# Performance work log

Measured on AMD Instinct MI355X. Metric: run time of the kernel, lower is better.

Reference implementation:

```python
import jax, jax.numpy as jnp
import numpy as np

B, CIN, COUT, N, TIN = 8, 64, 64, 207, 54
K, NHID, SL, KT = 8, 64, 3, 3
HEADS, STRIDE, PL = 8, 4, 8
TIME_NUM, OUT_LEN = 120, 48
E = COUT * PL            # 512 = attention embed dim (embed_size*patch_len)
PD = E // HEADS          # 64 per-head dim
PNUM = (OUT_LEN + STRIDE - PL) // STRIDE + 1   # 12 patches
EPS = 1e-5


def setup_inputs():
    keys = iter(jax.random.split(jax.random.key(0), 48))
    def rn(shape, s):
        return jax.random.normal(next(keys), shape, jnp.float32) * s
    d = {}
    d['x'] = rn((B, CIN, N, TIN), 1.0)
    d['adj'] = jax.random.uniform(next(keys), (SL, N, N), jnp.float32) / N
    d['W_conv1'] = rn((COUT, CIN), 0.125); d['b_conv1'] = rn((COUT,), 0.02)
    d['g_T'] = jnp.ones((TIN,), jnp.float32); d['b_T'] = jnp.zeros((TIN,), jnp.float32)
    d['g_S'] = jnp.ones((N,), jnp.float32); d['b_S'] = jnp.zeros((N,), jnp.float32)
    d['W_time'] = rn((2*COUT, 3*COUT, 1, KT), 1.0/np.sqrt(3*COUT*KT)); d['b_time'] = rn((2*COUT,), 0.02)
    d['wq1'] = rn((SL, K, COUT, NHID), 0.125); d['wv1'] = rn((SL, K, COUT, NHID), 0.125)
    d['bias1'] = rn((SL, NHID), 0.05)
    d['wq2'] = rn((SL, K, NHID, 2*COUT), 0.125); d['wv2'] = rn((SL, K, NHID, 2*COUT), 0.125)
    d['bias2'] = rn((SL, 2*COUT), 0.05)
    d['W_mlp'] = rn((2*COUT, SL*2*COUT, 1, KT), 1.0/np.sqrt(SL*2*COUT*KT)); d['b_mlp'] = rn((2*COUT,), 0.02)
    d['emb_T'] = rn((TIME_NUM, E), 0.02)
    d['Wq'] = rn((PD, PD), 0.125); d['bq'] = rn((PD,), 0.02)
    d['Wk'] = rn((PD, PD), 0.125); d['bk'] = rn((PD,), 0.02)
    d['Wv'] = rn((PD, PD), 0.125); d['bv'] = rn((PD,), 0.02)
    d['W_fc'] = rn((E, E), 1.0/np.sqrt(E)); d['b_fc'] = rn((E,), 0.02)
    d['g1'] = jnp.ones((E,), jnp.float32); d['b1n'] = jnp.zeros((E,), jnp.float32)
    d['g2'] = jnp.ones((E,), jnp.float32); d['b2n'] = jnp.zeros((E,), jnp.float32)
    d['W_ff1'] = rn((E, 4*COUT), 1.0/np.sqrt(E)); d['b_ff1'] = rn((4*COUT,), 0.02)
    d['W_ff2'] = rn((4*COUT, E), 1.0/np.sqrt(4*COUT)); d['b_ff2'] = rn((E,), 0.02)
    d['W_rp'] = rn((PNUM*PL, OUT_LEN), 1.0/np.sqrt(PNUM*PL)); d['b_rp'] = rn((OUT_LEN,), 0.02)
    d['g_bn'] = jnp.ones((COUT,), jnp.float32); d['b_bn'] = jnp.zeros((COUT,), jnp.float32)
    return d


def _ln(v, g, b, axis):
    m = jnp.mean(v, axis=axis, keepdims=True)
    var = jnp.var(v, axis=axis, keepdims=True)
    xhat = (v - m) * jax.lax.rsqrt(var + EPS)
    shp = [1] * v.ndim; shp[axis] = -1
    return xhat * g.reshape(shp) + b.reshape(shp)


def _gconv(x, wq, wv, bias, a):
    # x: [B,C,N,L]; wq/wv: [K,C,D]; a: [N,N]  -- multi-basis sigmoid-gated GCN
    q = jnp.einsum('bcnl,kcd->kbdnl', x, wq)
    v = jnp.einsum('bcnl,kcd->kbdnl', x, wv)
    s = jnp.sum(jax.nn.sigmoid(q) * v, axis=0)           # [B,D,N,L]
    out = jnp.einsum('nk,bcnl->bckl', a, s)              # adjacency aggregation (exact index order of source)
    return out + bias[None, :, None, None]


def _conv2d(x, w, b, dil):
    y = jax.lax.conv_general_dilated(x, w, (1, 1), 'VALID', rhs_dilation=(1, dil),
                                     dimension_numbers=('NCHW', 'OIHW', 'NCHW'))
    return y + b[None, :, None, None]


def reference(x, adj, W_conv1, b_conv1, g_T, b_T, g_S, b_S, W_time, b_time,
              wq1, wv1, bias1, wq2, wv2, bias2, W_mlp, b_mlp, emb_T,
              Wq, bq, Wk, bk, Wv, bv, W_fc, b_fc, g1, b1n, g2, b2n,
              W_ff1, b_ff1, W_ff2, b_ff2, W_rp, b_rp, g_bn, b_bn):
    residual = jnp.einsum('oc,bcnl->bonl', W_conv1, x) + b_conv1[None, :, None, None]
    xcat = jnp.concatenate([residual, _ln(residual, g_T, b_T, 3), _ln(residual, g_S, b_S, 2)], axis=1)
    h = _conv2d(xcat, W_time, b_time, 2)                 # [B,2C,N,50]
    h = jnp.tanh(h[:, :COUT]) * jax.nn.sigmoid(h[:, COUT:])
    outs = [_gconv(jax.nn.relu(_gconv(h, wq1[i], wv1[i], bias1[i], adj[i])),
                   wq2[i], wv2[i], bias2[i], adj[i]) for i in range(SL)]
    g = _conv2d(jnp.concatenate(outs, axis=1), W_mlp, b_mlp, 1)   # [B,2C,N,48]
    g = jnp.tanh(g[:, :COUT]) * jax.nn.sigmoid(g[:, COUT:])      # [B,C,N,48]
    # --- TTransformer with patching ---
    z = jnp.pad(g, ((0, 0), (0, 0), (0, 0), (0, STRIDE)))        # pad time by stride (52 >= patch_len)
    idx = jnp.arange(PNUM)[:, None] * STRIDE + jnp.arange(PL)[None, :]
    patches = z[..., idx]                                        # [B,C,N,P,PL] unfold
    q0 = patches.reshape(B, N, PNUM, E)                          # row-major reshape, as in torch source
    xe = q0 + emb_T[:PNUM][None, None]
    qh = xe.reshape(B, N, PNUM, HEADS, PD)
    qs = qh @ Wq + bq; ks = qh @ Wk + bk; vs = qh @ Wv + bv
    scores = jnp.einsum('bnqhd,bnkhd->bnqkh', qs, ks)
    att = jax.nn.softmax(scores / jnp.sqrt(jnp.float32(E)), axis=2)   # softmax over QUERY axis (faithful to source)
    ao = jnp.einsum('bnqkh,bnkhd->bnqhd', att, vs).reshape(B, N, PNUM, E) @ W_fc + b_fc
    M = _ln(ao + xe, g1, b1n, 3)
    ff = jax.nn.relu(M @ W_ff1 + b_ff1) @ W_ff2 + b_ff2
    U = _ln(M + ff, g2, b2n, 3)
    o = (U + xe + M).reshape(B, N, COUT, PNUM * PL) @ W_rp + b_rp     # [B,N,C,48]
    o = jnp.transpose(o, (0, 2, 1, 3))                               # [B,C,N,48]
    # --- BatchNorm2d (training-mode batch stats) over residual sum ---
    y = o + residual[..., -OUT_LEN:]
    m = jnp.mean(y, axis=(0, 2, 3), keepdims=True)
    var = jnp.var(y, axis=(0, 2, 3), keepdims=True)
    return (y - m) * jax.lax.rsqrt(var + EPS) * g_bn[None, :, None, None] + b_bn[None, :, None, None]
```

## Files before the change

### kernel.cpp

```cpp
#include <hip/hip_runtime.h>
#include <hip/hip_bf16.h>

#define TPB 256
#define TPA 512

constexpr int Bx = 8, Cc = 64, Nn = 207, Tin = 54, Kb = 8;
constexpr int LP = 52, NP = Nn * LP;
constexpr int NPa = 10816;
constexpr int L50 = 50, Tout = 48;
constexpr int Ee = 512, Pn = 12;
constexpr float EPSF = 1e-5f;
constexpr int SRDF = 516;

constexpr size_t O_RESID = 0;
constexpr size_t O_LNTM  = O_RESID + (size_t)Bx*Cc*Nn*Tin;
constexpr size_t O_LNTR  = O_LNTM  + (size_t)Bx*Cc*Nn;
constexpr size_t O_LNSM  = O_LNTR  + (size_t)Bx*Cc*Nn;
constexpr size_t O_LNSR  = O_LNSM  + (size_t)Bx*Cc*Tin;
constexpr size_t O_XCAT  = O_LNSR  + (size_t)Bx*Cc*Tin;
constexpr size_t O_RB    = O_XCAT  + (size_t)Bx*192*Nn*Tin;
constexpr size_t O_H     = O_RB    + (size_t)Bx*128*NP;
constexpr size_t O_GACC  = O_H     + (size_t)Bx*64*NP;
constexpr size_t O_GG    = O_GACC  + (size_t)Bx*128*Nn*Tout;
constexpr size_t O_XE    = O_GG    + (size_t)Bx*64*Nn*Tout;
constexpr size_t O_WTT   = O_XE    + (size_t)Bx*Nn*Pn*Ee;
constexpr size_t O_WTM   = O_WTT   + (size_t)128*192*3;
constexpr size_t O_BNST  = O_WTM   + (size_t)128*384*3;
constexpr size_t O_WTB   = O_BNST + 128;
constexpr size_t O_ADJT  = O_WTB  + (size_t)128*576/2;
constexpr size_t O_HT    = O_H;
constexpr size_t O_TAIL  = O_XCAT + (size_t)Bx*128*NP;
constexpr size_t O_WQ1B  = O_TAIL + (size_t)Bx*NPa*64/2;
constexpr size_t O_WV1B  = O_WQ1B + (size_t)24*64*64/2;
constexpr size_t O_WQ2B  = O_WV1B + (size_t)24*64*64/2;
constexpr size_t O_WV2B  = O_WQ2B + (size_t)24*128*64/2;
constexpr size_t O_RBT   = O_WV2B + (size_t)24*128*64/2;
constexpr size_t O_WQT   = O_RBT  + (size_t)Bx*NPa*64/2;
constexpr size_t O_WKT   = O_WQT  + 2048;
constexpr size_t O_WVT   = O_WKT  + 2048;
constexpr size_t O_WFCT  = O_WVT  + 2048;
constexpr size_t O_WF1T  = O_WFCT + 131072;
constexpr size_t O_WF2T  = O_WF1T + 65536;

#define FMA4(acc, sA_, vB_) { (acc).x += (sA_)*(vB_).x; (acc).y += (sA_)*(vB_).y; (acc).z += (sA_)*(vB_).z; (acc).w += (sA_)*(vB_).w; }

typedef __attribute__((ext_vector_type(8))) short bf16x8;
typedef __attribute__((ext_vector_type(4))) float f32x4;

__device__ __forceinline__ float sigm(float x){ return 1.0f/(1.0f+__expf(-x)); }
__device__ __forceinline__ ushort f2bf(float x){ __hip_bfloat16 h = __float2bfloat16(x); return *(ushort*)&h; }

__global__ __launch_bounds__(TPB) void k_residual(const float* __restrict__ x, const float* __restrict__ W,
                                                  const float* __restrict__ bias, float* __restrict__ out,
                                                  float* __restrict__ lnm, float* __restrict__ lnr){
  int n = blockIdx.x, b = blockIdx.y;
  __shared__ __align__(16) float sX[Cc][Tin];
  __shared__ __align__(16) float sW[Cc*Cc];
  __shared__ __align__(16) float sO[Cc][Tin];
  int tid = threadIdx.x;
  for(int i=tid;i<Cc*Tin;i+=TPB){ int c=i/Tin, l=i%Tin; sX[c][l] = x[((size_t)(b*Cc+c)*Nn+n)*Tin+l]; }
  for(int i=tid;i<Cc*Cc;i+=TPB) sW[i]=W[i];
  __syncthreads();
  for(int i=tid;i<Cc*Tin;i+=TPB){
    int o=i/Tin, l=i%Tin; float acc=bias[o];
    #pragma unroll 8
    for(int c=0;c<Cc;c++) acc += sW[o*Cc+c]*sX[c][l];
    out[((size_t)(b*Cc+o)*Nn+n)*Tin+l]=acc;
    sO[o][l]=acc;
  }
  __syncthreads();
  if(tid < Cc){
    float s=0.f,s2=0.f;
    for(int l=0;l<Tin;l++){ float v=sO[tid][l]; s+=v; s2+=v*v; }
    float m=s*(1.f/Tin); float var=s2*(1.f/Tin)-m*m;
    int row = (b*Cc+tid)*Nn + n;
    lnm[row]=m; lnr[row]=rsqrtf(fmaxf(var,0.f)+EPSF);
  }
}

__global__ __launch_bounds__(TPB) void k_lnS(const float* __restrict__ r, float* __restrict__ mean, float* __restrict__ rstd){
  int row = blockIdx.x*TPB + threadIdx.x;
  if(row >= Bx*Cc*Tin) return;
  int l = row % Tin; int bc = row / Tin;
  const float* p = r + (size_t)bc*Nn*Tin + l;
  float s=0.f,s2=0.f;
  for(int n=0;n<Nn;n++){ float v=p[(size_t)n*Tin]; s+=v; s2+=v*v; }
  float m=s*(1.f/Nn); float var=s2*(1.f/Nn)-m*m;
  mean[row]=m; rstd[row]=rsqrtf(fmaxf(var,0.f)+EPSF);
}

struct WJob { const float* W; ushort* F; int K, N, KS, NT, sStride, total; };
struct WJobs { WJob j[11]; };

__global__ __launch_bounds__(TPB) void k_wfrag_all(WJobs jobs){
  int gi = blockIdx.x*TPB + threadIdx.x;
  for(int seg=0; seg<11; seg++){
    const WJob J = jobs.j[seg];
    if(gi < J.total){
      int i = gi;
      int j = i & 7; int lane = (i>>3) & 63;
      int t = i >> 9;
      int ks = t % J.KS; int r = t / J.KS; int colTile = r % J.NT; int s = r / J.NT;
      int r15 = lane & 15, hi = lane >> 4;
      int k = ks*32 + hi*8 + j, col = colTile*16 + r15;
      float v = (k < J.K && col < J.N) ? J.W[(size_t)s*J.sStride + (size_t)k*J.N + col] : 0.f;
      J.F[i] = f2bf(v);
      return;
    }
    gi -= J.total;
  }
}

__global__ __launch_bounds__(TPB) void k_wtbF(const float* __restrict__ W, ushort* __restrict__ F){
  int i = blockIdx.x*TPB + threadIdx.x;
  if(i >= 8*18*512) return;
  int j = i & 7; int lane = (i>>3) & 63;
  int t = i >> 9;
  int ks = t % 18; int colTile = t / 18;
  int r15 = lane & 15, hi = lane >> 4;
  int k = ks*32 + hi*8 + j, o = colTile*16 + r15;
  int kt = k/192, ci = k - kt*192;
  F[i] = f2bf(W[(size_t)(o*192+ci)*3 + kt]);
}

__global__ __launch_bounds__(TPB) void k_wmlpF(const float* __restrict__ W, ushort* __restrict__ F){
  int i = blockIdx.x*TPB + threadIdx.x;
  if(i >= 3*8*12*512) return;
  int j = i & 7; int lane = (i>>3) & 63;
  int t = i >> 9;
  int ks = t % 12; int r = t / 12; int colTile = r & 7; int layer = r >> 3;
  int r15 = lane & 15, hi = lane >> 4;
  int k = ks*32 + hi*8 + j;
  int kt = k >> 7, ci = k & 127;
  int o = colTile*16 + r15;
  F[i] = f2bf(W[(size_t)(o*384 + layer*128 + ci)*3 + kt]);
}

__global__ __launch_bounds__(TPB) void k_timeconv_mfma(const float* __restrict__ resid,
    const float* __restrict__ tm, const float* __restrict__ tr,
    const float* __restrict__ sm, const float* __restrict__ sr,
    const float* __restrict__ gT, const float* __restrict__ bT,
    const float* __restrict__ gS, const float* __restrict__ bS,
    const ushort* __restrict__ WF, const float* __restrict__ bias, ushort* __restrict__ HT){
  int n = blockIdx.x, b = blockIdx.y;
  constexpr int XS = 200;
  __shared__ __align__(16) ushort sXT[68*XS];
  int tid = threadIdx.x;
  for(int i=tid; i<14*XS; i+=TPB) sXT[54*XS + i] = 0;
  float gSn = gS[n], bSn = bS[n];
  for(int i=tid; i<64*54; i+=TPB){
    int cm = i/54, l = i%54;
    int rowT = (b*Cc+cm)*Nn + n;
    float r = resid[(size_t)rowT*Tin + l];
    float v1 = (r - tm[rowT]) * tr[rowT] * gT[l] + bT[l];
    int rowS = (b*Cc+cm)*Tin + l;
    float v2 = (r - sm[rowS]) * sr[rowS] * gSn + bSn;
    sXT[l*XS + cm]        = f2bf(r);
    sXT[l*XS + 64 + cm]   = f2bf(v1);
    sXT[l*XS + 128 + cm]  = f2bf(v2);
  }
  __syncthreads();
  int lane = tid & 63, w = tid >> 6;
  int r15 = lane & 15, hi = lane >> 4;
  float b0 = bias[w*16 + r15], b1 = bias[w*16 + 64 + r15];
  f32x4 acc0[4], acc1[4];
  #pragma unroll
  for(int tt=0;tt<4;tt++){
    acc0[tt][0]=b0; acc0[tt][1]=b0; acc0[tt][2]=b0; acc0[tt][3]=b0;
    acc1[tt][0]=b1; acc1[tt][1]=b1; acc1[tt][2]=b1; acc1[tt][3]=b1;
  }
  const ushort* wp0 = WF + ((size_t)w*18)*512 + lane*8;
  const ushort* wp1 = WF + ((size_t)(w+4)*18)*512 + lane*8;
  #pragma unroll 2
  for(int ks=0; ks<18; ks++){
    int k0 = ks*32 + hi*8;
    int kt = k0/192, ci0 = k0 - kt*192;
    bf16x8 bw0 = *(const bf16x8*)&wp0[(size_t)ks*512];
    bf16x8 bw1 = *(const bf16x8*)&wp1[(size_t)ks*512];
    #pragma unroll
    for(int tt=0;tt<4;tt++){
      bf16x8 ax = *(const bf16x8*)&sXT[(tt*16 + r15 + 2*kt)*XS + ci0];
      acc0[tt] = __builtin_amdgcn_mfma_f32_16x16x32_bf16(ax, bw0, acc0[tt], 0,0,0);
      acc1[tt] = __builtin_amdgcn_mfma_f32_16x16x32_bf16(ax, bw1, acc1[tt], 0,0,0);
    }
  }
  ushort* htp = HT + ((size_t)b*NPa + (size_t)n*LP)*64;
  int c = w*16 + r15;
  #pragma unroll
  for(int tt=0;tt<4;tt++){
    int t0 = tt*16 + hi*4;
    #pragma unroll
    for(int i=0;i<4;i++){
      int t = t0 + i;
      if(t < L50) htp[(size_t)t*64 + c] = f2bf(tanhf(acc0[tt][i])*sigm(acc1[tt][i]));
    }
  }
  if(tid < 128){ int cz = tid >> 1, tz = 50 + (tid & 1); htp[(size_t)tz*64 + cz] = 0; }
}

__global__ __launch_bounds__(TPB) void k_htpad(ushort* __restrict__ HT){
  int i = blockIdx.x*TPB + threadIdx.x;
  int per = (NPa-NP)*8;
  if(i >= Bx*per) return;
  int b = i / per, r = i % per;
  uint4 z; z.x=0;z.y=0;z.z=0;z.w=0;
  *(uint4*)&HT[((size_t)b*NPa + NP)*64 + (size_t)r*8] = z;
}

template<int D, int TR>
__global__ __launch_bounds__(TPB) void k_gcs_mfma(const ushort* __restrict__ XT,
    const ushort* __restrict__ wqF, const ushort* __restrict__ wvF,
    ushort* __restrict__ S){
  constexpr int Dt = D/16;
  int p0 = blockIdx.x*64;
  int b = blockIdx.z;
  int tid = threadIdx.x;
  int lane = tid & 63, w = tid >> 6;
  int d0 = blockIdx.y*64 + (w<<4);
  int dTile = blockIdx.y*4 + w;
  __shared__ __align__(16) ushort sX[64*64];
  if constexpr(TR){
    __shared__ __align__(16) ushort sT2[64*66];
    for(int i=tid;i<4096;i+=TPB){ int c=i>>6, col=i&63; int p=p0+col;
      sT2[c*66+col] = (p<NP) ? XT[((size_t)(b*64+c))*NP + p] : (ushort)0; }
    __syncthreads();
    for(int i=tid;i<512;i+=TPB){
      int row=i>>3, c8=(i&7)<<3;
      ushort u[8];
      #pragma unroll
      for(int j=0;j<8;j++) u[j] = sT2[(c8+j)*66 + row];
      *(uint4*)&sX[row*64 + (c8 ^ ((row&7)<<3))] = *(uint4*)u;
    }
  } else {
    for(int i=tid;i<512;i+=TPB){
      int row=i>>3, c8=(i&7)<<3;
      uint4 v = *(const uint4*)&XT[((size_t)b*NPa + p0 + row)*64 + c8];
      *(uint4*)&sX[row*64 + (c8 ^ ((row&7)<<3))] = v;
    }
  }
  __syncthreads();
  int r15 = lane & 15, hi = lane >> 4;
  bf16x8 bf[4][2];
  #pragma unroll
  for(int pt=0;pt<4;pt++){
    int row = pt*16 + r15;
    int sw = (row&7)<<3;
    int cu0 = hi*8;
    bf[pt][0] = *(const bf16x8*)&sX[row*64 + (cu0 ^ sw)];
    bf[pt][1] = *(const bf16x8*)&sX[row*64 + ((cu0+32) ^ sw)];
  }
  f32x4 acc[4];
  #pragma unroll
  for(int pt=0;pt<4;pt++){ acc[pt][0]=0.f; acc[pt][1]=0.f; acc[pt][2]=0.f; acc[pt][3]=0.f; }
  const ushort* wqp = wqF + ((size_t)dTile*2)*512 + lane*8;
  const ushort* wvp = wvF + ((size_t)dTile*2)*512 + lane*8;
  for(int k=0;k<Kb;k++){
    bf16x8 aq0 = *(const bf16x8*)&wqp[0];
    bf16x8 aq1 = *(const bf16x8*)&wqp[512];
    bf16x8 av0 = *(const bf16x8*)&wvp[0];
    bf16x8 av1 = *(const bf16x8*)&wvp[512];
    wqp += (size_t)Dt*2*512; wvp += (size_t)Dt*2*512;
    #pragma unroll
    for(int pt=0;pt<4;pt++){
      f32x4 q; q[0]=0.f;q[1]=0.f;q[2]=0.f;q[3]=0.f;
      f32x4 v; v[0]=0.f;v[1]=0.f;v[2]=0.f;v[3]=0.f;
      q = __builtin_amdgcn_mfma_f32_16x16x32_bf16(aq0, bf[pt][0], q, 0,0,0);
      q = __builtin_amdgcn_mfma_f32_16x16x32_bf16(aq1, bf[pt][1], q, 0,0,0);
      v = __builtin_amdgcn_mfma_f32_16x16x32_bf16(av0, bf[pt][0], v, 0,0,0);
      v = __builtin_amdgcn_mfma_f32_16x16x32_bf16(av1, bf[pt][1], v, 0,0,0);
      #pragma unroll
      for(int i=0;i<4;i++) acc[pt][i] += v[i]*sigm(q[i]);
    }
  }
  #pragma unroll
  for(int pt=0;pt<4;pt++){
    int p = p0 + pt*16 + r15;
    if(p < NP){
      #pragma unroll
      for(int i=0;i<4;i++){
        int d = d0 + hi*4 + i;
        S[((size_t)b*D + d)*NP + p] = f2bf(acc[pt][i]);
      }
    }
  }
}

template<int RELU>
__global__ __launch_bounds__(TPB) void k_agg_mfma(const ushort* __restrict__ S, const ushort* __restrict__ adjF,
                                                  const float* __restrict__ bias, ushort* __restrict__ Out, int D){
  int d = blockIdx.x, b = blockIdx.y;
  int bd = b*D + d;
  constexpr int SST = 232;
  __shared__ __align__(16) ushort sB[64*SST];
  int tid = threadIdx.x;
  for(int i=tid*8; i<64*SST; i+=TPB*8){ uint4 z; z.x=0;z.y=0;z.z=0;z.w=0; *(uint4*)&sB[i]=z; }
  __syncthreads();
  const ushort* Sp = S + (size_t)bd*NP;
  for(int i=tid; i<NP; i+=TPB){
    int nn = i/52, l = i - nn*52;
    sB[l*SST + nn] = Sp[i];
  }
  __syncthreads();
  int lane = tid & 63, w = tid >> 6;
  int r15 = lane & 15, hi = lane >> 4;
  float bb = bias[d];
  ushort* Op = Out + (size_t)bd*NP;
  for(int k2t = w; k2t < 13; k2t += 4){
    f32x4 acc[4];
    #pragma unroll
    for(int lt=0;lt<4;lt++){ acc[lt][0]=0;acc[lt][1]=0;acc[lt][2]=0;acc[lt][3]=0; }
    #pragma unroll
    for(int ks=0; ks<7; ks++){
      bf16x8 a = *(const bf16x8*)&adjF[((size_t)(k2t*7 + ks))*512 + lane*8];
      #pragma unroll
      for(int lt=0;lt<4;lt++){
        bf16x8 bfr = *(const bf16x8*)&sB[(lt*16+r15)*SST + ks*32 + hi*8];
        acc[lt] = __builtin_amdgcn_mfma_f32_16x16x32_bf16(a, bfr, acc[lt], 0,0,0);
      }
    }
    #pragma unroll
    for(int lt=0;lt<4;lt++){
      #pragma unroll
      for(int i2=0;i2<4;i2++){
        int k2 = k2t*16 + hi*4 + i2;
        int l  = lt*16 + r15;
        if(k2 < Nn && l < LP){
          float v = acc[lt][i2] + bb;
          if(RELU) v = fmaxf(v, 0.f);
          Op[(size_t)k2*LP + l] = f2bf(v);
        }
      }
    }
  }
}

__global__ __launch_bounds__(TPB) void k_mlp_all(const ushort* __restrict__ RB0, const ushort* __restrict__ RB1,
                                                 const ushort* __restrict__ RB2, const ushort* __restrict__ WF,
                                                 const float* __restrict__ bm, float* __restrict__ gg){
  int n = blockIdx.x, b = blockIdx.y;
  constexpr int CS = 136;
  __shared__ __align__(16) ushort sLT[3*52*CS];
  int tid = threadIdx.x;
  {
    const ushort* Rp = RB0;
    for(int i=tid;i<6656;i+=TPB){ int c=i/52, l=i%52; sLT[0*52*CS + l*CS + c] = Rp[(((size_t)b*128+c)*Nn + n)*LP + l]; }
    Rp = RB1;
    for(int i=tid;i<6656;i+=TPB){ int c=i/52, l=i%52; sLT[1*52*CS + l*CS + c] = Rp[(((size_t)b*128+c)*Nn + n)*LP + l]; }
    Rp = RB2;
    for(int i=tid;i<6656;i+=TPB){ int c=i/52, l=i%52; sLT[2*52*CS + l*CS + c] = Rp[(((size_t)b*128+c)*Nn + n)*LP + l]; }
  }
  __syncthreads();
  int lane = tid & 63, w = tid >> 6;
  int r15 = lane & 15, hi = lane >> 4;
  f32x4 acc0[3], acc1[3];
  #pragma unroll
  for(int tt=0;tt<3;tt++){
    acc0[tt][0]=0;acc0[tt][1]=0;acc0[tt][2]=0;acc0[tt][3]=0;
    acc1[tt][0]=0;acc1[tt][1]=0;acc1[tt][2]=0;acc1[tt][3]=0;
  }
  #pragma unroll
  for(int layer=0; layer<3; layer++){
    const ushort* wp0 = WF + ((size_t)(layer*8 + w)*12)*512 + lane*8;
    const ushort* wp1 = WF + ((size_t)(layer*8 + w+4)*12)*512 + lane*8;
    const ushort* sL = &sLT[layer*52*CS];
    #pragma unroll 3
    for(int ks=0; ks<12; ks++){
      int kt = ks>>2, ci0 = (ks&3)*32 + hi*8;
      bf16x8 bw0 = *(const bf16x8*)&wp0[(size_t)ks*512];
      bf16x8 bw1 = *(const bf16x8*)&wp1[(size_t)ks*512];
      #pragma unroll
      for(int tt=0;tt<3;tt++){
        bf16x8 ax = *(const bf16x8*)&sL[(tt*16 + r15 + kt)*CS + ci0];
        acc0[tt] = __builtin_amdgcn_mfma_f32_16x16x32_bf16(ax, bw0, acc0[tt], 0,0,0);
        acc1[tt] = __builtin_amdgcn_mfma_f32_16x16x32_bf16(ax, bw1, acc1[tt], 0,0,0);
      }
    }
  }
  int o = w*16 + r15;
  float b0 = bm[o], b1 = bm[o+64];
  float* ggp = gg + (((size_t)b*Cc + o)*Nn + n)*(size_t)Tout;
  #pragma unroll
  for(int tt=0;tt<3;tt++){
    #pragma unroll
    for(int i2=0;i2<4;i2++){
      int tq = tt*16 + hi*4 + i2;
      float a  = acc0[tt][i2] + b0;
      float g2 = acc1[tt][i2] + b1;
      ggp[tq] = tanhf(a)*sigm(g2);
    }
  }
}

__global__ __launch_bounds__(TPB) void k_xe(const float* __restrict__ gg, const float* __restrict__ emb, float* __restrict__ xe){
  size_t i = (size_t)blockIdx.x*TPB + threadIdx.x;
  if(i >= (size_t)Bx*1271808) return;
  int b = (int)(i / 1271808);
  int off = (int)(i % 1271808);
  int c = off / 19872; int r = off % 19872;
  int n = r / 96; int r2 = r % 96;
  int p = r2 >> 3; int j = r2 & 7;
  int t = p*4 + j;
  float v = 0.f;
  if(t < Tout) v = gg[(((size_t)b*Cc+c)*Nn + n)*Tout + t];
  int e = off & 511; int p2 = (off >> 9) % 12;
  xe[i] = v + emb[(size_t)p2*Ee + e];
}

template<int NW>
__device__ __forceinline__ void ln_rows(float* buf, const float* __restrict__ g, const float* __restrict__ be, int tid){
  int lane = tid & 63, wv = tid >> 6;
  for(int r = wv; r < 12; r += NW){
    float s=0.f, s2=0.f;
    #pragma unroll
    for(int j=0;j<8;j++){ float v = buf[r*SRDF + j*64 + lane]; s+=v; s2+=v*v; }
    #pragma unroll
    for(int off=32; off; off>>=1){ s += __shfl_xor(s,off); s2 += __shfl_xor(s2,off); }
    float m = s*(1.f/512.f);
    float rstd = rsqrtf(fmaxf(s2*(1.f/512.f)-m*m, 0.f)+EPSF);
    #pragma unroll
    for(int j=0;j<8;j++){ int e = j*64+lane; float v = buf[r*SRDF+e];
      buf[r*SRDF+e] = (v-m)*rstd*g[e] + be[e]; }
  }
}

__global__ __launch_bounds__(TPA,2) void k_attn(
    const float* __restrict__ xe, const float* __restrict__ resid,
    const ushort* __restrict__ WqF, const float* __restrict__ bq,
    const ushort* __restrict__ WkF, const float* __restrict__ bk,
    const ushort* __restrict__ WvF, const float* __restrict__ bv,
    const ushort* __restrict__ WfcF, const float* __restrict__ bfc,
    const float* __restrict__ g1, const float* __restrict__ b1n,
    const float* __restrict__ g2, const float* __restrict__ b2n,
    const ushort* __restrict__ Wff1F, const float* __restrict__ bff1,
    const ushort* __restrict__ Wff2F, const float* __restrict__ bff2,
    const float* __restrict__ Wrp, const float* __restrict__ brp,
    float* __restrict__ y)
{
  int n = blockIdx.x, b = blockIdx.y;
  __shared__ __align__(16) ushort SbX[16*512];
  __shared__ __align__(16) ushort Mb[16*256];
  __shared__ __align__(16) float U0[12*SRDF];
  __shared__ __align__(16) float U1[12*SRDF];
  __shared__ __align__(16) float sS[1160];
  int tid = threadIdx.x;
  int lane = tid & 63, w = tid >> 6;
  int r15 = lane & 15, hi = lane >> 4;
  const float* __restrict__ xeg = xe + ((size_t)b*Nn + n)*6144;

  for(int i=tid;i<1024;i+=TPA){
    int r = i>>6, ch = i&63;
    ushort u[8];
    if(r<12){
      const float* s = &xeg[r*512 + ch*8];
      #pragma unroll
      for(int j=0;j<8;j++) u[j] = f2bf(s[j]);
    } else {
      #pragma unroll
      for(int j=0;j<8;j++) u[j] = 0;
    }
    *(uint4*)&SbX[r*512 + ((ch ^ (r&7))<<3)] = *(uint4*)u;
  }
  for(int i=tid;i<128;i+=TPA){
    int r = 12 + (i>>5), ch = i&31;
    uint4 z; z.x=0;z.y=0;z.z=0;z.w=0;
    *(uint4*)&Mb[r*256 + ch*8] = z;
  }
  __syncthreads();

  f32x4 vfrag[4];
  {
    int head = w;
    bf16x8 a0, a1;
    { int ch0 = head*8 + hi, ch1 = head*8 + 4 + hi;
      a0 = *(const bf16x8*)&SbX[r15*512 + ((ch0 ^ (r15&7))<<3)];
      a1 = *(const bf16x8*)&SbX[r15*512 + ((ch1 ^ (r15&7))<<3)]; }
    #pragma unroll
    for(int nt=0;nt<4;nt++){
      int col = nt*16 + r15;
      float bb = bq[col];
      f32x4 acc; acc[0]=bb;acc[1]=bb;acc[2]=bb;acc[3]=bb;
      acc = __builtin_amdgcn_mfma_f32_16x16x32_bf16(a0, *(const bf16x8*)&WqF[(size_t)(nt*2+0)*512 + lane*8], acc, 0,0,0);
      acc = __builtin_amdgcn_mfma_f32_16x16x32_bf16(a1, *(const bf16x8*)&WqF[(size_t)(nt*2+1)*512 + lane*8], acc, 0,0,0);
      #pragma unroll
      for(int i2=0;i2<4;i2++){ int p = hi*4+i2; if(p<12) U0[p*SRDF + head*64 + col] = acc[i2]; }
    }
    #pragma unroll
    for(int nt=0;nt<4;nt++){
      int col = nt*16 + r15;
      float bb = bk[col];
      f32x4 acc; acc[0]=bb;acc[1]=bb;acc[2]=bb;acc[3]=bb;
      acc = __builtin_amdgcn_mfma_f32_16x16x32_bf16(a0, *(const bf16x8*)&WkF[(size_t)(nt*2+0)*512 + lane*8], acc, 0,0,0);
      acc = __builtin_amdgcn_mfma_f32_16x16x32_bf16(a1, *(const bf16x8*)&WkF[(size_t)(nt*2+1)*512 + lane*8], acc, 0,0,0);
      #pragma unroll
      for(int i2=0;i2<4;i2++){ int p = hi*4+i2; if(p<12) U1[p*SRDF + head*64 + col] = acc[i2]; }
    }
    #pragma unroll
    for(int nt=0;nt<4;nt++){
      int col = nt*16 + r15;
      float bb = bv[col];
      f32x4 acc; acc[0]=bb;acc[1]=bb;acc[2]=bb;acc[3]=bb;
      acc = __builtin_amdgcn_mfma_f32_16x16x32_bf16(a0, *(const bf16x8*)&WvF[(size_t)(nt*2+0)*512 + lane*8], acc, 0,0,0);
      acc = __builtin_amdgcn_mfma_f32_16x16x32_bf16(a1, *(const bf16x8*)&WvF[(size_t)(nt*2+1)*512 + lane*8], acc, 0,0,0);
      vfrag[nt] = acc;
    }
  }
  __syncthreads();

  const float scale = 0.04419417382415922f;
  for(int i=tid;i<1152;i+=TPA){
    int q = i%12, kh = i/12; int h2 = kh&7, k2 = kh>>3;
    const float* qp = &U0[q*SRDF + h2*64];
    const float* kp = &U1[k2*SRDF + h2*64];
    float s=0.f;
    #pragma unroll
    for(int d4=0; d4<16; d4++){
      float4 a4 = *(const float4*)&qp[d4*4];
      float4 b4 = *(const float4*)&kp[d4*4];
      s += a4.x*b4.x + a4.y*b4.y + a4.z*b4.z + a4.w*b4.w;
    }
    sS[i] = s*scale;
  }
  __syncthreads();
  {
    int head = w;
    #pragma unroll
    for(int nt=0;nt<4;nt++){
      int col = nt*16 + r15;
      #pragma unroll
      for(int i2=0;i2<4;i2++){ int p = hi*4+i2; if(p<12) U0[p*SRDF + head*64 + col] = vfrag[nt][i2]; }
    }
  }
  if(tid<96){
    float mx=-1e30f;
    for(int q=0;q<12;q++) mx = fmaxf(mx, sS[tid*12+q]);
    float sm=0.f;
    for(int q=0;q<12;q++){ float e = __expf(sS[tid*12+q]-mx); sS[tid*12+q]=e; sm+=e; }
    float inv = 1.f/sm;
    for(int q=0;q<12;q++) sS[tid*12+q] *= inv;
  }
  __syncthreads();

  for(int i=tid;i<6144;i+=TPA){
    int q=i>>9, h2=(i>>6)&7, d=i&63;
    float s=0.f;
    #pragma unroll
    for(int k2=0;k2<12;k2++) s += sS[(k2*8+h2)*12+q]*U0[k2*SRDF+h2*64+d];
    int kk = i & 511;
    SbX[q*512 + (((kk>>3) ^ (q&7))<<3) + (kk&7)] = f2bf(s);
  }
  __syncthreads();

  {
    f32x4 acc[4];
    #pragma unroll
    for(int nt=0;nt<4;nt++){ float bb = bfc[(w*4+nt)*16 + r15]; acc[nt][0]=bb;acc[nt][1]=bb;acc[nt][2]=bb;acc[nt][3]=bb; }
    for(int ks=0;ks<16;ks++){
      int ch = ks*4 + hi;
      bf16x8 a = *(const bf16x8*)&SbX[r15*512 + ((ch ^ (r15&7))<<3)];
      #pragma unroll
      for(int nt=0;nt<4;nt++){
        acc[nt] = __builtin_amdgcn_mfma_f32_16x16x32_bf16(a, *(const bf16x8*)&WfcF[(size_t)((w*4+nt)*16 + ks)*512 + lane*8], acc[nt], 0,0,0);
      }
    }
    #pragma unroll
    for(int nt=0;nt<4;nt++){
      int col = (w*4+nt)*16 + r15;
      #pragma unroll
      for(int i2=0;i2<4;i2++){ int p = hi*4+i2; if(p<12) U1[p*SRDF + col] = acc[nt][i2] + xeg[p*512 + col]; }
    }
  }
  __syncthreads();
  ln_rows<8>(U1, g1, b1n, tid);
  __syncthreads();

  for(int i=tid;i<6144;i+=TPA){
    int r=i>>9, kk=i&511;
    SbX[r*512 + (((kk>>3) ^ (r&7))<<3) + (kk&7)] = f2bf(U1[r*SRDF + kk]);
  }
  __syncthreads();

  {
    f32x4 acc[2];
    #pragma unroll
    for(int nt=0;nt<2;nt++){ float bb = bff1[(w*2+nt)*16 + r15]; acc[nt][0]=bb;acc[nt][1]=bb;acc[nt][2]=bb;acc[nt][3]=bb; }
    for(int ks=0;ks<16;ks++){
      int ch = ks*4 + hi;
      bf16x8 a = *(const bf16x8*)&SbX[r15*512 + ((ch ^ (r15&7))<<3)];
      #pragma unroll
      for(int nt=0;nt<2;nt++){
        acc[nt] = __builtin_amdgcn_mfma_f32_16x16x32_bf16(a, *(const bf16x8*)&Wff1F[(size_t)((w*2+nt)*16 + ks)*512 + lane*8], acc[nt], 0,0,0);
      }
    }
    #pragma unroll
    for(int nt=0;nt<2;nt++){
      int u = (w*2+nt)*16 + r15;
      #pragma unroll
      for(int i2=0;i2<4;i2++){
        int p = hi*4+i2;
        if(p<12) Mb[p*256 + (((u>>3) ^ (p&7))<<3) + (u&7)] = f2bf(fmaxf(acc[nt][i2], 0.f));
      }
    }
  }
  __syncthreads();

  {
    f32x4 acc[4];
    #pragma unroll
    for(int nt=0;nt<4;nt++){ float bb = bff2[(w*4+nt)*16 + r15]; acc[nt][0]=bb;acc[nt][1]=bb;acc[nt][2]=bb;acc[nt][3]=bb; }
    for(int ks=0;ks<8;ks++){
      int ch = ks*4 + hi;
      bf16x8 a = *(const bf16x8*)&Mb[r15*256 + ((ch ^ (r15&7))<<3)];
      #pragma unroll
      for(int nt=0;nt<4;nt++){
        acc[nt] = __builtin_amdgcn_mfma_f32_16x16x32_bf16(a, *(const bf16x8*)&Wff2F[(size_t)((w*4+nt)*8 + ks)*512 + lane*8], acc[nt], 0,0,0);
      }
    }
    #pragma unroll
    for(int nt=0;nt<4;nt++){
      int col = (w*4+nt)*16 + r15;
      #pragma unroll
      for(int i2=0;i2<4;i2++){ int p = hi*4+i2; if(p<12) U0[p*SRDF + col] = acc[nt][i2] + U1[p*SRDF + col]; }
    }
  }
  __syncthreads();
  ln_rows<8>(U0, g2, b2n, tid);
  __syncthreads();

  for(int i=tid;i<6144;i+=TPA){
    int r=i>>9, c=i&511;
    U1[r*SRDF+c] = U0[r*SRDF+c] + U1[r*SRDF+c] + xeg[r*512+c];
  }
  __syncthreads();
  for(int i=tid;i<4608;i+=TPA) U0[i] = Wrp[i];
  __syncthreads();
  #pragma unroll
  for(int j=0;j<2;j++){
    int i4 = tid + j*TPA;
    if(i4 < 768){
      int c = i4/12, tq = i4%12; int t0 = tq*4;
      float4 acc = *(const float4*)&brp[t0];
      for(int t96=0;t96<96;t96++){
        int f = c*96 + t96;
        float a = U1[(f>>9)*SRDF + (f&511)];
        float4 w4 = *(const float4*)&U0[t96*48 + t0];
        FMA4(acc, a, w4);
      }
      size_t rb = (((size_t)b*Cc+c)*Nn + n)*Tin + 6 + t0;
      acc.x += resid[rb+0]; acc.y += resid[rb+1]; acc.z += resid[rb+2]; acc.w += resid[rb+3];
      *(float4*)&y[(((size_t)b*Cc+c)*Nn + n)*Tout + t0] = acc;
    }
  }
}

__global__ __launch_bounds__(TPB) void k_bnstats(const float* __restrict__ y, float* __restrict__ stats){
  int c = blockIdx.x; int tid = threadIdx.x;
  float s=0.f,s2=0.f;
  const int per = Nn*Tout;
  for(int idx=tid; idx<Bx*per; idx+=TPB){
    int b = idx/per, r = idx%per;
    float v = y[((size_t)b*Cc+c)*per + r];
    s+=v; s2+=v*v;
  }
  __shared__ float rs[TPB], rs2[TPB];
  rs[tid]=s; rs2[tid]=s2; __syncthreads();
  for(int off=TPB/2; off; off>>=1){ if(tid<off){ rs[tid]+=rs[tid+off]; rs2[tid]+=rs2[tid+off]; } __syncthreads(); }
  if(tid==0){
    float m = rs[0]/(float)(Bx*per);
    float var = rs2[0]/(float)(Bx*per) - m*m;
    stats[c]=m; stats[64+c]=rsqrtf(fmaxf(var,0.f)+EPSF);
  }
}
__global__ __launch_bounds__(TPB) void k_bnout(const float* __restrict__ y, const float* __restrict__ stats,
                                               const float* __restrict__ gbn, const float* __restrict__ bbn,
                                               float* __restrict__ out){
  size_t i = (size_t)blockIdx.x*TPB + threadIdx.x;
  if(i >= (size_t)Bx*Cc*Nn*Tout) return;
  int c = (int)((i/(Nn*Tout))%Cc);
  out[i] = (y[i]-stats[c])*stats[64+c]*gbn[c] + bbn[c];
}

extern "C" void kernel_launch(void* const* d_in, const int* in_sizes, int n_in,
                              void* d_out, int out_size, void* d_ws, size_t ws_size,
                              hipStream_t stream) {
  const float* x      = (const float*)d_in[0];
  const float* adj    = (const float*)d_in[1];
  const float* Wconv1 = (const float*)d_in[2];
  const float* bconv1 = (const float*)d_in[3];
  const float* gT     = (const float*)d_in[4];
  const float* bT     = (const float*)d_in[5];
  const float* gS     = (const float*)d_in[6];
  const float* bS     = (const float*)d_in[7];
  const float* Wtime  = (const float*)d_in[8];
  const float* btime  = (const float*)d_in[9];
  const float* wq1    = (const float*)d_in[10];
  const float* wv1    = (const float*)d_in[11];
  const float* bias1  = (const float*)d_in[12];
  const float* wq2    = (const float*)d_in[13];
  const float* wv2    = (const float*)d_in[14];
  const float* bias2  = (const float*)d_in[15];
  const float* Wmlp   = (const float*)d_in[16];
  const float* bmlp   = (const float*)d_in[17];
  const float* embT   = (const float*)d_in[18];
  const float* Wq     = (const float*)d_in[19];
  const float* bq     = (const float*)d_in[20];
  const float* Wk     = (const float*)d_in[21];
  const float* bk     = (const float*)d_in[22];
  const float* Wv     = (const float*)d_in[23];
  const float* bv     = (const float*)d_in[24];
  const float* Wfc    = (const float*)d_in[25];
  const float* bfc    = (const float*)d_in[26];
  const float* g1     = (const float*)d_in[27];
  const float* b1n    = (const float*)d_in[28];
  const float* g2     = (const float*)d_in[29];
  const float* b2n    = (const float*)d_in[30];
  const float* Wff1   = (const float*)d_in[31];
  const float* bff1   = (const float*)d_in[32];
  const float* Wff2   = (const float*)d_in[33];
  const float* bff2   = (const float*)d_in[34];
  const float* Wrp    = (const float*)d_in[35];
  const float* brp    = (const float*)d_in[36];
  const float* gbn    = (const float*)d_in[37];
  const float* bbn    = (const float*)d_in[38];

  float* ws = (float*)d_ws;
  float* RESID = ws + O_RESID;
  float* LNTM  = ws + O_LNTM;
  float* LNTR  = ws + O_LNTR;
  float* LNSM  = ws + O_LNSM;
  float* LNSR  = ws + O_LNSR;
  ushort* RA   = (ushort*)(ws + O_XCAT);
  ushort* RB2  = RA + (size_t)Bx*128*NP;
  ushort* RB0  = (ushort*)(ws + O_RB);
  ushort* RB1  = RB0 + (size_t)Bx*128*NP;
  ushort* S1   = (ushort*)(ws + O_GACC);
  float* GG    = ws + O_GG;
  float* Y     = ws + O_GG;
  float* XE    = ws + O_XE;
  float* BNST  = ws + O_BNST;
  ushort* WTMF = (ushort*)(ws + O_WTM);
  ushort* WTB  = (ushort*)(ws + O_WTB);
  ushort* ADJT = (ushort*)(ws + O_ADJT);
  ushort* HT   = (ushort*)(ws + O_HT);
  ushort* WQ1B = (ushort*)(ws + O_WQ1B);
  ushort* WV1B = (ushort*)(ws + O_WV1B);
  ushort* WQ2B = (ushort*)(ws + O_WQ2B);
  ushort* WV2B = (ushort*)(ws + O_WV2B);
  ushort* WQT  = (ushort*)(ws + O_WQT);
  ushort* WKT  = (ushort*)(ws + O_WKT);
  ushort* WVT  = (ushort*)(ws + O_WVT);
  ushort* WFCT = (ushort*)(ws + O_WFCT);
  ushort* WF1T = (ushort*)(ws + O_WF1T);
  ushort* WF2T = (ushort*)(ws + O_WF2T);

  k_residual<<<dim3(Nn,Bx),TPB,0,stream>>>(x, Wconv1, bconv1, RESID, LNTM, LNTR);
  k_lnS<<<(Bx*Cc*Tin)/TPB,TPB,0,stream>>>(RESID, LNSM, LNSR);
  k_wtbF<<<(8*18*512+TPB-1)/TPB,TPB,0,stream>>>(Wtime, WTB);
  k_wmlpF<<<(3*8*12*512+TPB-1)/TPB,TPB,0,stream>>>(Wmlp, WTMF);
  k_htpad<<<(Bx*(NPa-NP)*8+TPB-1)/TPB,TPB,0,stream>>>(HT);
  k_timeconv_mfma<<<dim3(Nn,Bx),TPB,0,stream>>>(RESID, LNTM, LNTR, LNSM, LNSR, gT, bT, gS, bS,
                                                WTB, btime, HT);

  WJobs jobs;
  jobs.j[0]  = { wq1,  WQ1B, 64,  64,  2,  4,  64*64,   24*4*2*512 };
  jobs.j[1]  = { wv1,  WV1B, 64,  64,  2,  4,  64*64,   24*4*2*512 };
  jobs.j[2]  = { wq2,  WQ2B, 64,  128, 2,  8,  64*128,  24*8*2*512 };
  jobs.j[3]  = { wv2,  WV2B, 64,  128, 2,  8,  64*128,  24*8*2*512 };
  jobs.j[4]  = { Wq,   WQT,  64,  64,  2,  4,  64*64,   4*2*512 };
  jobs.j[5]  = { Wk,   WKT,  64,  64,  2,  4,  64*64,   4*2*512 };
  jobs.j[6]  = { Wv,   WVT,  64,  64,  2,  4,  64*64,   4*2*512 };
  jobs.j[7]  = { Wfc,  WFCT, 512, 512, 16, 32, 512*512, 32*16*512 };
  jobs.j[8]  = { Wff1, WF1T, 512, 256, 16, 16, 512*256, 16*16*512 };
  jobs.j[9]  = { Wff2, WF2T, 256, 512, 8,  32, 256*512, 32*8*512 };
  jobs.j[10] = { adj,  ADJT, 207, 207, 7,  13, Nn*Nn,   3*13*7*512 };
  int totalW = 2*(24*4*2*512) + 2*(24*8*2*512) + 3*(4*2*512) + 32*16*512 + 16*16*512 + 32*8*512 + 3*13*7*512;
  k_wfrag_all<<<(totalW+TPB-1)/TPB,TPB,0,stream>>>(jobs);

  ushort* RBv[3] = { RB0, RB1, RB2 };
  for(int i=0;i<3;i++){
    k_gcs_mfma<64,0><<<dim3(169,1,Bx),TPB,0,stream>>>(HT, WQ1B+(size_t)i*8*4*2*512, WV1B+(size_t)i*8*4*2*512, RA);
    k_agg_mfma<1><<<dim3(64,Bx),TPB,0,stream>>>(RA, ADJT+(size_t)i*13*7*512, bias1+(size_t)i*64, S1, 64);
    k_gcs_mfma<128,1><<<dim3(169,2,Bx),TPB,0,stream>>>(S1, WQ2B+(size_t)i*8*8*2*512, WV2B+(size_t)i*8*8*2*512, RA);
    k_agg_mfma<0><<<dim3(128,Bx),TPB,0,stream>>>(RA, ADJT+(size_t)i*13*7*512, bias2+(size_t)i*128, RBv[i], 128);
  }
  k_mlp_all<<<dim3(Nn,Bx),TPB,0,stream>>>(RB0, RB1, RB2, WTMF, bmlp, GG);
  k_xe<<<(Bx*1271808)/TPB,TPB,0,stream>>>(GG, embT, XE);
  k_attn<<<dim3(Nn,Bx),TPA,0,stream>>>(XE, RESID, WQT,bq, WKT,bk, WVT,bv, WFCT,bfc,
                                       g1,b1n,g2,b2n, WF1T,bff1, WF2T,bff2, Wrp,brp, Y);
  k_bnstats<<<64,TPB,0,stream>>>(Y, BNST);
  k_bnout<<<(Bx*Cc*Nn*Tout)/TPB,TPB,0,stream>>>(Y, BNST, gbn, bbn, (float*)d_out);
}
```

Measured before the change: 858.5 us.

## Batch the three graph-conv layers into single launches over a layer grid dimension

Replaces the per-layer loop of 12 small kernel launches with 4 launches whose grid covers all three support layers, indexing weights, adjacency, bias and buffers by a layer index. Workspace is reorganised so each layer gets its own intermediate slot, and RB2 is placed in the XE region. This removes launch overhead and the serialisation between layers so more blocks run concurrently, at the cost of a larger intermediate footprint and reuse of the XE buffer before k_xe writes it.

```diff
diff --git a/kernel.cpp b/kernel.cpp
--- a/kernel.cpp
+++ b/kernel.cpp
@@ -29,13 +29,11 @@
 constexpr size_t O_WTB   = O_BNST + 128;
 constexpr size_t O_ADJT  = O_WTB  + (size_t)128*576/2;
 constexpr size_t O_HT    = O_H;
-constexpr size_t O_TAIL  = O_XCAT + (size_t)Bx*128*NP;
-constexpr size_t O_WQ1B  = O_TAIL + (size_t)Bx*NPa*64/2;
-constexpr size_t O_WV1B  = O_WQ1B + (size_t)24*64*64/2;
-constexpr size_t O_WQ2B  = O_WV1B + (size_t)24*64*64/2;
-constexpr size_t O_WV2B  = O_WQ2B + (size_t)24*128*64/2;
-constexpr size_t O_RBT   = O_WV2B + (size_t)24*128*64/2;
-constexpr size_t O_WQT   = O_RBT  + (size_t)Bx*NPa*64/2;
+constexpr size_t O_WQ1B  = O_ADJT + (size_t)3*13*7*512/2;
+constexpr size_t O_WV1B  = O_WQ1B + (size_t)24*4*2*512/2;
+constexpr size_t O_WQ2B  = O_WV1B + (size_t)24*4*2*512/2;
+constexpr size_t O_WV2B  = O_WQ2B + (size_t)24*8*2*512/2;
+constexpr size_t O_WQT   = O_WV2B + (size_t)24*8*2*512/2;
 constexpr size_t O_WKT   = O_WQT  + 2048;
 constexpr size_t O_WVT   = O_WKT  + 2048;
 constexpr size_t O_WFCT  = O_WVT  + 2048;
@@ -210,19 +208,27 @@
 template<int D, int TR>
 __global__ __launch_bounds__(TPB) void k_gcs_mfma(const ushort* __restrict__ XT,
     const ushort* __restrict__ wqF, const ushort* __restrict__ wvF,
-    ushort* __restrict__ S){
+    ushort* __restrict__ S, size_t inSlot, size_t outSlot){
   constexpr int Dt = D/16;
+  constexpr int nY = D/64;
+  constexpr size_t WSTR = (size_t)Kb*Dt*2*512;
   int p0 = blockIdx.x*64;
   int b = blockIdx.z;
+  int iy = blockIdx.y / nY;
+  int dblk = blockIdx.y % nY;
   int tid = threadIdx.x;
   int lane = tid & 63, w = tid >> 6;
-  int d0 = blockIdx.y*64 + (w<<4);
-  int dTile = blockIdx.y*4 + w;
+  int d0 = dblk*64 + (w<<4);
+  int dTile = dblk*4 + w;
+  const ushort* wqB = wqF + iy*WSTR;
+  const ushort* wvB = wvF + iy*WSTR;
+  ushort* Sb = S + iy*outSlot;
   __shared__ __align__(16) ushort sX[64*64];
   if constexpr(TR){
+    const ushort* Xp = XT + iy*inSlot;
     __shared__ __align__(16) ushort sT2[64*66];
     for(int i=tid;i<4096;i+=TPB){ int c=i>>6, col=i&63; int p=p0+col;
-      sT2[c*66+col] = (p<NP) ? XT[((size_t)(b*64+c))*NP + p] : (ushort)0; }
+      sT2[c*66+col] = (p<NP) ? Xp[((size_t)(b*64+c))*NP + p] : (ushort)0; }
     __syncthreads();
     for(int i=tid;i<512;i+=TPB){
       int row=i>>3, c8=(i&7)<<3;
@@ -252,8 +258,8 @@
   f32x4 acc[4];
   #pragma unroll
   for(int pt=0;pt<4;pt++){ acc[pt][0]=0.f; acc[pt][1]=0.f; acc[pt][2]=0.f; acc[pt][3]=0.f; }
-  const ushort* wqp = wqF + ((size_t)dTile*2)*512 + lane*8;
-  const ushort* wvp = wvF + ((size_t)dTile*2)*512 + lane*8;
+  const ushort* wqp = wqB + ((size_t)dTile*2)*512 + lane*8;
+  const ushort* wvp = wvB + ((size_t)dTile*2)*512 + lane*8;
   for(int k=0;k<Kb;k++){
     bf16x8 aq0 = *(const bf16x8*)&wqp[0];
     bf16x8 aq1 = *(const bf16x8*)&wqp[512];
@@ -279,7 +285,7 @@
       #pragma unroll
       for(int i=0;i<4;i++){
         int d = d0 + hi*4 + i;
-        S[((size_t)b*D + d)*NP + p] = f2bf(acc[pt][i]);
+        Sb[((size_t)b*D + d)*NP + p] = f2bf(acc[pt][i]);
       }
     }
   }
@@ -287,15 +293,20 @@
 
 template<int RELU>
 __global__ __launch_bounds__(TPB) void k_agg_mfma(const ushort* __restrict__ S, const ushort* __restrict__ adjF,
-                                                  const float* __restrict__ bias, ushort* __restrict__ Out, int D){
-  int d = blockIdx.x, b = blockIdx.y;
+                                                  const float* __restrict__ bias,
+                                                  ushort* __restrict__ O0, ushort* __restrict__ O1, ushort* __restrict__ O2,
+                                                  int D, size_t inSlot){
+  int d = blockIdx.x;
+  int by = blockIdx.y;
+  int b = by / 3, li = by % 3;
   int bd = b*D + d;
+  const ushort* adjL = adjF + (size_t)li*13*7*512;
   constexpr int SST = 232;
   __shared__ __align__(16) ushort sB[64*SST];
   int tid = threadIdx.x;
   for(int i=tid*8; i<64*SST; i+=TPB*8){ uint4 z; z.x=0;z.y=0;z.z=0;z.w=0; *(uint4*)&sB[i]=z; }
   __syncthreads();
-  const ushort* Sp = S + (size_t)bd*NP;
+  const ushort* Sp = S + li*inSlot + (size_t)bd*NP;
   for(int i=tid; i<NP; i+=TPB){
     int nn = i/52, l = i - nn*52;
     sB[l*SST + nn] = Sp[i];
@@ -303,15 +314,16 @@
   __syncthreads();
   int lane = tid & 63, w = tid >> 6;
   int r15 = lane & 15, hi = lane >> 4;
-  float bb = bias[d];
-  ushort* Op = Out + (size_t)bd*NP;
+  float bb = bias[li*D + d];
+  ushort* Ob = (li==0) ? O0 : (li==1 ? O1 : O2);
+  ushort* Op = Ob + (size_t)bd*NP;
   for(int k2t = w; k2t < 13; k2t += 4){
     f32x4 acc[4];
     #pragma unroll
     for(int lt=0;lt<4;lt++){ acc[lt][0]=0;acc[lt][1]=0;acc[lt][2]=0;acc[lt][3]=0; }
     #pragma unroll
     for(int ks=0; ks<7; ks++){
-      bf16x8 a = *(const bf16x8*)&adjF[((size_t)(k2t*7 + ks))*512 + lane*8];
+      bf16x8 a = *(const bf16x8*)&adjL[((size_t)(k2t*7 + ks))*512 + lane*8];
       #pragma unroll
       for(int lt=0;lt<4;lt++){
         bf16x8 bfr = *(const bf16x8*)&sB[(lt*16+r15)*SST + ks*32 + hi*8];
@@ -728,11 +740,13 @@
   float* LNTR  = ws + O_LNTR;
   float* LNSM  = ws + O_LNSM;
   float* LNSR  = ws + O_LNSR;
-  ushort* RA   = (ushort*)(ws + O_XCAT);
-  ushort* RB2  = RA + (size_t)Bx*128*NP;
+  const size_t RSLOT  = (size_t)Bx*128*NP;
+  const size_t S1SLOT = (size_t)Bx*64*NP;
+  ushort* RAx  = (ushort*)(ws + O_XCAT);
   ushort* RB0  = (ushort*)(ws + O_RB);
-  ushort* RB1  = RB0 + (size_t)Bx*128*NP;
-  ushort* S1   = (ushort*)(ws + O_GACC);
+  ushort* RB1  = RB0 + RSLOT;
+  ushort* RB2  = (ushort*)(ws + O_XE);
+  ushort* S1x  = (ushort*)(ws + O_GACC);
   float* GG    = ws + O_GG;
   float* Y     = ws + O_GG;
   float* XE    = ws + O_XE;
@@ -775,13 +789,10 @@
   int totalW = 2*(24*4*2*512) + 2*(24*8*2*512) + 3*(4*2*512) + 32*16*512 + 16*16*512 + 32*8*512 + 3*13*7*512;
   k_wfrag_all<<<(totalW+TPB-1)/TPB,TPB,0,stream>>>(jobs);
 
-  ushort* RBv[3] = { RB0, RB1, RB2 };
-  for(int i=0;i<3;i++){
-    k_gcs_mfma<64,0><<<dim3(169,1,Bx),TPB,0,stream>>>(HT, WQ1B+(size_t)i*8*4*2*512, WV1B+(size_t)i*8*4*2*512, RA);
-    k_agg_mfma<1><<<dim3(64,Bx),TPB,0,stream>>>(RA, ADJT+(size_t)i*13*7*512, bias1+(size_t)i*64, S1, 64);
-    k_gcs_mfma<128,1><<<dim3(169,2,Bx),TPB,0,stream>>>(S1, WQ2B+(size_t)i*8*8*2*512, WV2B+(size_t)i*8*8*2*512, RA);
-    k_agg_mfma<0><<<dim3(128,Bx),TPB,0,stream>>>(RA, ADJT+(size_t)i*13*7*512, bias2+(size_t)i*128, RBv[i], 128);
-  }
+  k_gcs_mfma<64,0><<<dim3(169,3,Bx),TPB,0,stream>>>(HT, WQ1B, WV1B, RAx, 0, RSLOT);
+  k_agg_mfma<1><<<dim3(64,Bx*3),TPB,0,stream>>>(RAx, ADJT, bias1, S1x, S1x+S1SLOT, S1x+2*S1SLOT, 64, RSLOT);
+  k_gcs_mfma<128,1><<<dim3(169,6,Bx),TPB,0,stream>>>(S1x, WQ2B, WV2B, RAx, S1SLOT, RSLOT);
+  k_agg_mfma<0><<<dim3(128,Bx*3),TPB,0,stream>>>(RAx, ADJT, bias2, RB0, RB1, RB2, 128, RSLOT);
   k_mlp_all<<<dim3(Nn,Bx),TPB,0,stream>>>(RB0, RB1, RB2, WTMF, bmlp, GG);
   k_xe<<<(Bx*1271808)/TPB,TPB,0,stream>>>(GG, embT, XE);
   k_attn<<<dim3(Nn,Bx),TPA,0,stream>>>(XE, RESID, WQT,bq, WKT,bk, WVT,bv, WFCT,bfc,
```

Result: faster. 797.7 us (-7.1%).
